# Kernel optimization log

Measured on AMD Instinct MI355X. Metric: run time of the kernel, lower is better.

## Reference

```python
import jax, jax.numpy as jnp
import numpy as np
from jax import lax

# ---- config (mirrors cfg) ----
NUM_LEVELS = 4
DS = 2            # DS_FACTOR
T = 16            # TILE_SIZE
SR = 4            # SEARCH_RADIUS
PADD = 1
SW = 0.1          # SPATIAL_WEIGHT
GR = 2            # GAUSS_RADIUS
SIGMA = 1.0
SS = 2 * (SR + PADD) + 1      # 11: padded search grid
SSC = 2 * SR + 1              # 9: cropped search grid
WIN = T + 2 * (SR + PADD)     # 26: gathered window per tile

# ---- subpixel-refinement quadratic-fit filters (from __init__) ----
F_A11 = jnp.asarray(np.array([[1,-2,1],[2,-4,2],[1,-2,1]], np.float32) / 4.0)
F_A22 = jnp.asarray(np.array([[1,2,1],[-2,-4,-2],[1,2,1]], np.float32) / 4.0)
F_A12 = jnp.asarray(np.array([[1,0,-1],[0,0,0],[-1,0,1]], np.float32) / 4.0)
F_B1  = jnp.asarray(np.array([[-1,0,1],[-2,0,2],[-1,0,1]], np.float32) / 8.0)
F_B2  = jnp.asarray(np.array([[-1,-2,-1],[0,0,0],[1,2,1]], np.float32) / 8.0)
F_C   = jnp.asarray(np.array([[-1,2,-1],[2,12,2],[-1,2,-1]], np.float32) / 16.0)


def _gauss_kernel():
    ws = 2 * GR + 1
    ax = np.arange(ws, dtype=np.float32) - GR
    g = np.exp(-(ax ** 2) / (2.0 * SIGMA ** 2))
    k = np.outer(g, g)
    k = k / k.sum()
    return jnp.asarray(k, jnp.float32)


def _pyramid(x):
    """Gaussian pyramid: depthwise gaussian blur + avg-pool(ds) per level."""
    k = _gauss_kernel()[None, None]  # OIHW, C=1
    pad = (2 * GR + 1 - 1) // 2
    pyr = [x]
    for _ in range(NUM_LEVELS - 1):
        y = lax.conv_general_dilated(x, k, (1, 1), [(pad, pad), (pad, pad)],
                                     dimension_numbers=('NCHW', 'OIHW', 'NCHW'))
        n, c, h, w = y.shape
        x = y.reshape(n, c, h // DS, DS, w // DS, DS).mean(axis=(3, 5))
        pyr.append(x)
    return pyr


def _sdist_map():
    ax = (np.arange(SS, dtype=np.float32) - (SR + PADD)) / float(SS)
    return jnp.asarray(ax[:, None] ** 2 + ax[None, :] ** 2, jnp.float32)


def _step(init_offset, src, dst):
    """One pyramid-level block-matching step + subpixel refine."""
    n, nth, ntw, _ = init_offset.shape
    H, W = src.shape[2], src.shape[3]
    oy = jnp.round(init_offset[..., 0]).astype(jnp.int32)
    ox = jnp.round(init_offset[..., 1]).astype(jnp.int32)
    base_y = (jnp.arange(nth, dtype=jnp.int32) * T)[None, :, None]
    base_x = (jnp.arange(ntw, dtype=jnp.int32) * T)[None, None, :]
    y0 = base_y + oy - (SR + PADD)
    x0 = base_x + ox - (SR + PADD)
    Y = jnp.clip(y0[..., None] + jnp.arange(WIN), 0, H - 1)
    X = jnp.clip(x0[..., None] + jnp.arange(WIN), 0, W - 1)
    nidx = jnp.arange(n)[:, None, None, None, None]
    window = dst[:, 0][nidx, Y[..., :, None], X[..., None, :]]
    # source tiles [n,nth,ntw,T,T]
    src_t = src[:, 0].reshape(n, nth, T, ntw, T).transpose(0, 1, 3, 2, 4)
    # all SSxSS candidate tiles from the window (static slide indices)
    sl = jnp.arange(SS)[:, None] + jnp.arange(T)[None, :]  # [SS,T]
    cand = window[:, :, :, sl[:, None, :, None], sl[None, :, None, :]]  # [n,nth,ntw,SS,SS,T,T]
    adist = jnp.mean((cand - src_t[:, :, :, None, None]) ** 2, axis=(-2, -1))
    dist_full = adist + SW * _sdist_map()  # [n,nth,ntw,SS,SS]
    dist = dist_full[:, :, :, PADD:-PADD, PADD:-PADD].reshape(n, nth, ntw, SSC * SSC)
    min_dist = jnp.min(dist, axis=3)
    pk = jnp.argmin(dist, axis=3)
    py = pk // SSC
    px = pk % SSC
    offset = init_offset + jnp.stack([(py - SR).astype(jnp.float32),
                                      (px - SR).astype(jnp.float32)], axis=3)
    # RegionSelection: 3x3 neighborhood of dist_full around (py+PADD, px+PADD)
    ry = (py + PADD)[..., None] + jnp.arange(-1, 2)
    rx = (px + PADD)[..., None] + jnp.arange(-1, 2)
    tyi = jnp.arange(nth)[None, :, None, None, None]
    txi = jnp.arange(ntw)[None, None, :, None, None]
    yreg = dist_full[nidx, tyi, txi, ry[..., :, None], rx[..., None, :]]  # [n,nth,ntw,3,3]
    s = lambda f: jnp.sum(f * yreg, axis=(-2, -1))
    a11 = jax.nn.relu(s(F_A11))
    a22 = jax.nn.relu(s(F_A22))
    a12 = s(F_A12)
    b1 = s(F_B1)
    b2 = s(F_B2)
    det = a11 * a22 - a12 ** 2
    a12z = jnp.where(det < 0, jnp.zeros_like(a12), a12)
    mu_x = -(a22 * b1 - a12z * b2) / det
    mu_y = -(a11 * b2 - a12z * b1) / det
    mu_len = jnp.sqrt(mu_y ** 2 + mu_x ** 2)
    dx = jnp.where(mu_len < 1.0, mu_x, jnp.zeros_like(mu_x))
    dy = jnp.where(mu_len < 1.0, mu_y, jnp.zeros_like(mu_y))
    offset = offset.at[..., 0].add(dy).at[..., 1].add(dx)
    return offset, min_dist


def _inherit(prev_offset, nth, ntw, H, W):
    typ = jnp.arange(nth) // DS
    txp = jnp.arange(ntw) // DS
    off = DS * prev_offset[:, typ[:, None], txp[None, :], :]
    iy = (jnp.arange(nth, dtype=jnp.float32) * T)[None, :, None]
    ix = (jnp.arange(ntw, dtype=jnp.float32) * T)[None, None, :]
    dy = jnp.clip(off[..., 0] + iy, 0.0, float(H - T)) - iy
    dx = jnp.clip(off[..., 1] + ix, 0.0, float(W - T)) - ix
    return jnp.round(jnp.stack([dy, dx], axis=3))


def _align(src, dst):
    ps = _pyramid(src)
    pd = _pyramid(dst)
    offset = None
    min_dist = None
    for level in range(NUM_LEVELS - 1, -1, -1):
        s, d = ps[level], pd[level]
        n, _, h, w = s.shape
        nth = int(np.ceil(h / T))
        ntw = int(np.ceil(w / T))
        if level == NUM_LEVELS - 1:
            init = jnp.zeros((n, nth, ntw, 2), jnp.float32)
        else:
            init = _inherit(offset, nth, ntw, h, w)
        offset, min_dist = _step(init, s, d)
    # nearest-neighbor upsample by TILE_SIZE to per-pixel maps
    pixel_off = jnp.repeat(jnp.repeat(offset, T, axis=1), T, axis=2)   # [n,H,W,2]
    pixel_dist = jnp.repeat(jnp.repeat(min_dist, T, axis=1), T, axis=2)  # [n,H,W]
    return pixel_off, pixel_dist


def setup_inputs() -> dict:
    key = jax.random.key(0)
    k1, k2 = jax.random.split(key)
    src = jax.random.uniform(k1, (4, 1, 512, 512), jnp.float32)
    dst = jax.random.uniform(k2, (4, 1, 512, 512), jnp.float32)
    return {"src": src, "dst": dst}


def reference(src, dst):
    return _align(src, dst)
```

## Files before the change

kernel.cpp:

```cpp
#include <hip/hip_runtime.h>


#define NB 4
#define NPIX (NB * 512 * 512)

constexpr float H6[6] = {
    0.027244342f, 0.149345013f, 0.323410645f,
    0.323410645f, 0.149345013f, 0.027244342f
};

__global__ void __launch_bounds__(256, 4)
pyramid_kernel(const float* __restrict__ src, const float* __restrict__ dst,
               float* __restrict__ ws) {
    __shared__ float smem[5520];
    float* patch = smem;
    float* tmpH1 = smem + 3840;
    float* l1    = smem;
    float* tmpH2 = smem + 784;
    float* l2    = smem + 1120;
    float* tmpH3 = smem + 1264;

    float* sL1 = ws;
    float* dL1 = sL1 + 4 * 65536;
    float* sL2 = dL1 + 4 * 65536;
    float* dL2 = sL2 + 4 * 16384;
    float* sL3 = dL2 + 4 * 16384;
    float* dL3 = sL3 + 4 * 4096;

    const int bx = blockIdx.x, by = blockIdx.y, z = blockIdx.z;
    const int t = threadIdx.x;
    const float* in = (z < 4) ? (src + (size_t)z * 262144) : (dst + (size_t)(z - 4) * 262144);
    float* oL1 = ((z < 4) ? sL1 : dL1) + (size_t)(z & 3) * 65536;
    float* oL2 = ((z < 4) ? sL2 : dL2) + (size_t)(z & 3) * 16384;
    float* oL3 = ((z < 4) ? sL3 : dL3) + (size_t)(z & 3) * 4096;

    {
        const int oy = by * 32 - 14, ox = bx * 32 - 14;
        for (int idx = t; idx < 3600; idx += 256) {
            int r = idx / 60, c = idx - r * 60;
            int gy = oy + r, gx = ox + c;
            float v = 0.f;
            if ((unsigned)gy < 512u && (unsigned)gx < 512u) v = in[gy * 512 + gx];
            patch[r * 64 + c] = v;
        }
    }
    __syncthreads();
    for (int idx = t; idx < 1680; idx += 256) {
        int r = idx / 28, v = idx - r * 28;
        const float* p = &patch[r * 64 + 2 * v];
        float a = 0.f;
        #pragma unroll
        for (int bq = 0; bq < 6; ++bq) a = fmaf(H6[bq], p[bq], a);
        tmpH1[r * 28 + v] = a;
    }
    __syncthreads();
    {
        const int oy = by * 16 - 6, ox = bx * 16 - 6;
        for (int idx = t; idx < 784; idx += 256) {
            int u = idx / 28, v = idx - u * 28;
            float a = 0.f;
            int y1 = oy + u, x1 = ox + v;
            if ((unsigned)y1 < 256u && (unsigned)x1 < 256u) {
                #pragma unroll
                for (int bq = 0; bq < 6; ++bq) a = fmaf(H6[bq], tmpH1[(2 * u + bq) * 28 + v], a);
            }
            l1[u * 28 + v] = a;
        }
    }
    __syncthreads();
    {
        int u = t >> 4, v = t & 15;
        oL1[(by * 16 + u) * 256 + bx * 16 + v] = l1[(6 + u) * 28 + 6 + v];
    }
    for (int idx = t; idx < 336; idx += 256) {
        int r = idx / 12, v = idx - r * 12;
        const float* p = &l1[r * 28 + 2 * v];
        float a = 0.f;
        #pragma unroll
        for (int bq = 0; bq < 6; ++bq) a = fmaf(H6[bq], p[bq], a);
        tmpH2[r * 12 + v] = a;
    }
    __syncthreads();
    {
        const int oy = by * 8 - 2, ox = bx * 8 - 2;
        if (t < 144) {
            int u = t / 12, v = t - u * 12;
            float a = 0.f;
            int y2 = oy + u, x2 = ox + v;
            if ((unsigned)y2 < 128u && (unsigned)x2 < 128u) {
                #pragma unroll
                for (int bq = 0; bq < 6; ++bq) a = fmaf(H6[bq], tmpH2[(2 * u + bq) * 12 + v], a);
            }
            l2[u * 12 + v] = a;
        }
    }
    __syncthreads();
    if (t < 64) {
        int u = t >> 3, v = t & 7;
        oL2[(by * 8 + u) * 128 + bx * 8 + v] = l2[(2 + u) * 12 + 2 + v];
    } else if (t < 112) {
        int idx = t - 64;
        int r = idx >> 2, v = idx & 3;
        const float* p = &l2[r * 12 + 2 * v];
        float a = 0.f;
        #pragma unroll
        for (int bq = 0; bq < 6; ++bq) a = fmaf(H6[bq], p[bq], a);
        tmpH3[r * 4 + v] = a;
    }
    __syncthreads();
    if (t < 16) {
        int u = t >> 2, v = t & 3;
        float a = 0.f;
        #pragma unroll
        for (int bq = 0; bq < 6; ++bq) a = fmaf(H6[bq], tmpH3[(2 * u + bq) * 4 + v], a);
        oL3[(by * 4 + u) * 64 + bx * 4 + v] = a;
    }
}

template<int NL>
__device__ __forceinline__ void do_level(const float* __restrict__ simg,
                                         const float* __restrict__ dimg, int H,
                                         int ty, int tx, float pary, float parx, bool first,
                                         float* win, float* st, float* dist, int lt,
                                         float& roy, float& rox, float& rod) {
    constexpr int ROWS = (NL == 128) ? 2 : 1;
    constexpr int G    = (NL == 128) ? 8 : 16;

    float dyf = 0.f, dxf = 0.f;
    if (!first) {
        float iy = (float)(ty * 16), ix = (float)(tx * 16);
        dyf = rintf(fminf(fmaxf(2.f * pary + iy, 0.f), (float)(H - 16)) - iy);
        dxf = rintf(fminf(fmaxf(2.f * parx + ix, 0.f), (float)(H - 16)) - ix);
    }
    const int ioy = (int)dyf, iox = (int)dxf;
    const int y0 = ty * 16 + ioy - 5;
    const int x0 = tx * 16 + iox - 5;

    for (int idx = lt; idx < 676; idx += NL) {
        int r = idx / 26, c = idx - r * 26;
        int gy = min(max(y0 + r, 0), H - 1);
        int gx = min(max(x0 + c, 0), H - 1);
        win[r * 28 + c] = dimg[gy * H + gx];
    }
    if (lt < 64) {
        int r = lt >> 2, q = lt & 3;
        const float4* srow = (const float4*)(simg + (size_t)(ty * 16 + r) * H + tx * 16);
        ((float4*)&st[r * 16])[q] = srow[q];
    }
    __syncthreads();

    const int dy = lt / G;
    if (dy < 11) {
        float acc[11];
        #pragma unroll
        for (int q = 0; q < 11; ++q) acc[q] = 0.f;
        #pragma unroll
        for (int rr = 0; rr < ROWS; ++rr) {
            const int i = (NL == 128) ? ((lt & 7) * 2 + rr) : (lt & 15);
            float w[28], s[16];
            const float4* wp = (const float4*)&win[(dy + i) * 28];
            #pragma unroll
            for (int q = 0; q < 7; ++q) ((float4*)w)[q] = wp[q];
            const float4* sp = (const float4*)&st[i * 16];
            #pragma unroll
            for (int q = 0; q < 4; ++q) ((float4*)s)[q] = sp[q];
            #pragma unroll
            for (int dx = 0; dx < 11; ++dx) {
                #pragma unroll
                for (int j = 0; j < 16; ++j) {
                    float d = w[dx + j] - s[j];
                    acc[dx] = fmaf(d, d, acc[dx]);
                }
            }
        }
        #pragma unroll
        for (int m = 1; m <= G / 2; m <<= 1) {
            #pragma unroll
            for (int dx = 0; dx < 11; ++dx) acc[dx] += __shfl_xor(acc[dx], m);
        }
        if ((lt & (G - 1)) == 0) {
            float ay = (float)(dy - 5) * (1.f / 11.f);
            #pragma unroll
            for (int dx = 0; dx < 11; ++dx) {
                float ax = (float)(dx - 5) * (1.f / 11.f);
                dist[dy * 11 + dx] = acc[dx] * (1.f / 256.f) + 0.1f * (ay * ay + ax * ax);
            }
        }
    }
    __syncthreads();

    const int l = lt & 63;
    float bv; int bk;
    {
        int k = l;
        int py = k / 9, px = k - (k / 9) * 9;
        bv = dist[(py + 1) * 11 + (px + 1)]; bk = k;
        k = l + 64;
        if (k < 81) {
            py = k / 9; px = k - (k / 9) * 9;
            float d = dist[(py + 1) * 11 + (px + 1)];
            if (d < bv) { bv = d; bk = k; }
        }
    }
    #pragma unroll
    for (int m = 1; m <= 32; m <<= 1) {
        float ov = __shfl_xor(bv, m);
        int   ok = __shfl_xor(bk, m);
        if (ov < bv || (ov == bv && ok < bk)) { bv = ov; bk = ok; }
    }
    {
        int py = bk / 9, px = bk - (bk / 9) * 9;
        float y00 = dist[(py + 0) * 11 + (px + 0)], y01 = dist[(py + 0) * 11 + (px + 1)], y02 = dist[(py + 0) * 11 + (px + 2)];
        float y10 = dist[(py + 1) * 11 + (px + 0)], y11 = dist[(py + 1) * 11 + (px + 1)], y12 = dist[(py + 1) * 11 + (px + 2)];
        float y20 = dist[(py + 2) * 11 + (px + 0)], y21 = dist[(py + 2) * 11 + (px + 1)], y22 = dist[(py + 2) * 11 + (px + 2)];

        float a11 = (y00 - 2.f * y01 + y02 + 2.f * y10 - 4.f * y11 + 2.f * y12 + y20 - 2.f * y21 + y22) * 0.25f;
        a11 = fmaxf(a11, 0.f);
        float a22 = (y00 + 2.f * y01 + y02 - 2.f * y10 - 4.f * y11 - 2.f * y12 + y20 + 2.f * y21 + y22) * 0.25f;
        a22 = fmaxf(a22, 0.f);
        float a12 = (y00 - y02 - y20 + y22) * 0.25f;
        float b1  = (-y00 + y02 - 2.f * y10 + 2.f * y12 - y20 + y22) * 0.125f;
        float b2  = (-y00 - 2.f * y01 - y02 + y20 + 2.f * y21 + y22) * 0.125f;

        float det  = a11 * a22 - a12 * a12;
        float a12z = (det < 0.f) ? 0.f : a12;
        float mu_x = -(a22 * b1 - a12z * b2) / det;
        float mu_y = -(a11 * b2 - a12z * b1) / det;
        float mu_len = sqrtf(mu_x * mu_x + mu_y * mu_y);
        float addx = (mu_len < 1.f) ? mu_x : 0.f;
        float addy = (mu_len < 1.f) ? mu_y : 0.f;

        roy = dyf + (float)(py - 4) + addy;
        rox = dxf + (float)(px - 4) + addx;
        rod = bv;
    }
}

__global__ void __launch_bounds__(512, 4)
step_chain_kernel(const float* __restrict__ src, const float* __restrict__ dst,
                  const float* __restrict__ ws, float* __restrict__ out) {
    __shared__ float smem[4448];

    const float* sL1 = ws;
    const float* dL1 = sL1 + 4 * 65536;
    const float* sL2 = dL1 + 4 * 65536;
    const float* dL2 = sL2 + 4 * 16384;
    const float* sL3 = dL2 + 4 * 16384;
    const float* dL3 = sL3 + 4 * 4096;

    const int gid = blockIdx.x;
    const int b   = gid >> 8;
    const int ty1 = (gid >> 4) & 15;
    const int tx1 = gid & 15;
    const int t    = threadIdx.x;
    const int slot = t >> 7;
    const int s_t  = t & 127;

    float* win0  = smem;
    float* st0   = smem + 2912;
    float* dist0 = smem + 3936;
    float* winH  = smem + slot * 728;
    float* stH   = smem + 2912 + slot * 256;
    float* distH = smem + 3936 + slot * 128;

    const float* s0 = src + (size_t)b * 262144; const float* d0 = dst + (size_t)b * 262144;
    const float* s1 = sL1 + (size_t)b * 65536;  const float* d1 = dL1 + (size_t)b * 65536;
    const float* s2 = sL2 + (size_t)b * 16384;  const float* d2 = dL2 + (size_t)b * 16384;
    const float* s3 = sL3 + (size_t)b * 4096;   const float* d3 = dL3 + (size_t)b * 4096;

    float oy, ox, od;
    do_level<512>(s3, d3,  64, ty1 >> 2, tx1 >> 2, 0.f, 0.f, true,
                  win0, st0, dist0, t, oy, ox, od);
    do_level<512>(s2, d2, 128, ty1 >> 1, tx1 >> 1, oy, ox, false,
                  win0, st0, dist0, t, oy, ox, od);
    do_level<512>(s1, d1, 256, ty1,      tx1,      oy, ox, false,
                  win0, st0, dist0, t, oy, ox, od);

    const int ty0 = 2 * ty1 + (slot >> 1), tx0 = 2 * tx1 + (slot & 1);
    do_level<128>(s0, d0, 512, ty0, tx0, oy, ox, false,
                  winH, stH, distH, s_t, oy, ox, od);

    int r = s_t >> 3, c = (s_t & 7) * 2;
    int pyy = ty0 * 16 + r, pxx = tx0 * 16 + c;
    size_t pi = ((size_t)(b * 512 + pyy)) * 512 + pxx;
    float2 o; o.x = oy; o.y = ox;
    ((float2*)out)[pi]     = o;
    ((float2*)out)[pi + 1] = o;
    float2 dd; dd.x = od; dd.y = od;
    *(float2*)(out + (size_t)NPIX * 2 + pi) = dd;
}

extern "C" void kernel_launch(void* const* d_in, const int* in_sizes, int n_in,
                              void* d_out, int out_size, void* d_ws, size_t ws_size,
                              hipStream_t stream) {
    const float* src = (const float*)d_in[0];
    const float* dst = (const float*)d_in[1];
    float* out = (float*)d_out;
    float* ws  = (float*)d_ws;

    hipLaunchKernelGGL(pyramid_kernel, dim3(16, 16, 8), dim3(256), 0, stream, src, dst, ws);
    hipLaunchKernelGGL(step_chain_kernel, dim3(1024), dim3(512), 0, stream, src, dst, ws, out);
}
```

Before: 117.4 us.

## Run one level-0 tile per 128-thread block, recomputing coarse levels redundantly

The step chain kernel now launches 4096 blocks of 128 threads, one per finest-level tile. Each block redundantly recomputes the coarse levels 3, 2 and 1 for its own ancestor tiles, instead of 512-thread blocks sharing those levels and splitting level 0 across four slots. The aim is more and smaller blocks with less shared memory, for better occupancy and less barrier cost. The cost is roughly four times the coarse-level work, and the coarse levels now use the 2-rows-per-thread path.

```diff
diff --git a/kernel.cpp b/kernel.cpp
--- a/kernel.cpp
+++ b/kernel.cpp
@@ -117,15 +117,11 @@
     }
 }
 
-template<int NL>
 __device__ __forceinline__ void do_level(const float* __restrict__ simg,
                                          const float* __restrict__ dimg, int H,
                                          int ty, int tx, float pary, float parx, bool first,
                                          float* win, float* st, float* dist, int lt,
                                          float& roy, float& rox, float& rod) {
-    constexpr int ROWS = (NL == 128) ? 2 : 1;
-    constexpr int G    = (NL == 128) ? 8 : 16;
-
     float dyf = 0.f, dxf = 0.f;
     if (!first) {
         float iy = (float)(ty * 16), ix = (float)(tx * 16);
@@ -136,7 +132,7 @@
     const int y0 = ty * 16 + ioy - 5;
     const int x0 = tx * 16 + iox - 5;
 
-    for (int idx = lt; idx < 676; idx += NL) {
+    for (int idx = lt; idx < 676; idx += 128) {
         int r = idx / 26, c = idx - r * 26;
         int gy = min(max(y0 + r, 0), H - 1);
         int gx = min(max(x0 + c, 0), H - 1);
@@ -149,14 +145,14 @@
     }
     __syncthreads();
 
-    const int dy = lt / G;
+    const int dy = lt >> 3;
     if (dy < 11) {
         float acc[11];
         #pragma unroll
         for (int q = 0; q < 11; ++q) acc[q] = 0.f;
         #pragma unroll
-        for (int rr = 0; rr < ROWS; ++rr) {
-            const int i = (NL == 128) ? ((lt & 7) * 2 + rr) : (lt & 15);
+        for (int rr = 0; rr < 2; ++rr) {
+            const int i = (lt & 7) * 2 + rr;
             float w[28], s[16];
             const float4* wp = (const float4*)&win[(dy + i) * 28];
             #pragma unroll
@@ -174,11 +170,11 @@
             }
         }
         #pragma unroll
-        for (int m = 1; m <= G / 2; m <<= 1) {
+        for (int m = 1; m <= 4; m <<= 1) {
             #pragma unroll
             for (int dx = 0; dx < 11; ++dx) acc[dx] += __shfl_xor(acc[dx], m);
         }
-        if ((lt & (G - 1)) == 0) {
+        if ((lt & 7) == 0) {
             float ay = (float)(dy - 5) * (1.f / 11.f);
             #pragma unroll
             for (int dx = 0; dx < 11; ++dx) {
@@ -236,10 +232,13 @@
     }
 }
 
-__global__ void __launch_bounds__(512, 4)
+__global__ void __launch_bounds__(128, 8)
 step_chain_kernel(const float* __restrict__ src, const float* __restrict__ dst,
                   const float* __restrict__ ws, float* __restrict__ out) {
-    __shared__ float smem[4448];
+    __shared__ float smem[1112];
+    float* win  = smem;
+    float* st   = smem + 728;
+    float* dist = smem + 984;
 
     const float* sL1 = ws;
     const float* dL1 = sL1 + 4 * 65536;
@@ -249,19 +248,10 @@
     const float* dL3 = sL3 + 4 * 4096;
 
     const int gid = blockIdx.x;
-    const int b   = gid >> 8;
-    const int ty1 = (gid >> 4) & 15;
-    const int tx1 = gid & 15;
-    const int t    = threadIdx.x;
-    const int slot = t >> 7;
-    const int s_t  = t & 127;
-
-    float* win0  = smem;
-    float* st0   = smem + 2912;
-    float* dist0 = smem + 3936;
-    float* winH  = smem + slot * 728;
-    float* stH   = smem + 2912 + slot * 256;
-    float* distH = smem + 3936 + slot * 128;
+    const int b   = gid >> 10;
+    const int ty0 = (gid >> 5) & 31;
+    const int tx0 = gid & 31;
+    const int t   = threadIdx.x;
 
     const float* s0 = src + (size_t)b * 262144; const float* d0 = dst + (size_t)b * 262144;
     const float* s1 = sL1 + (size_t)b * 65536;  const float* d1 = dL1 + (size_t)b * 65536;
@@ -269,18 +259,16 @@
     const float* s3 = sL3 + (size_t)b * 4096;   const float* d3 = dL3 + (size_t)b * 4096;
 
     float oy, ox, od;
-    do_level<512>(s3, d3,  64, ty1 >> 2, tx1 >> 2, 0.f, 0.f, true,
-                  win0, st0, dist0, t, oy, ox, od);
-    do_level<512>(s2, d2, 128, ty1 >> 1, tx1 >> 1, oy, ox, false,
-                  win0, st0, dist0, t, oy, ox, od);
-    do_level<512>(s1, d1, 256, ty1,      tx1,      oy, ox, false,
-                  win0, st0, dist0, t, oy, ox, od);
-
-    const int ty0 = 2 * ty1 + (slot >> 1), tx0 = 2 * tx1 + (slot & 1);
-    do_level<128>(s0, d0, 512, ty0, tx0, oy, ox, false,
-                  winH, stH, distH, s_t, oy, ox, od);
-
-    int r = s_t >> 3, c = (s_t & 7) * 2;
+    do_level(s3, d3,  64, ty0 >> 3, tx0 >> 3, 0.f, 0.f, true,
+             win, st, dist, t, oy, ox, od);
+    do_level(s2, d2, 128, ty0 >> 2, tx0 >> 2, oy, ox, false,
+             win, st, dist, t, oy, ox, od);
+    do_level(s1, d1, 256, ty0 >> 1, tx0 >> 1, oy, ox, false,
+             win, st, dist, t, oy, ox, od);
+    do_level(s0, d0, 512, ty0,      tx0,      oy, ox, false,
+             win, st, dist, t, oy, ox, od);
+
+    int r = t >> 3, c = (t & 7) * 2;
     int pyy = ty0 * 16 + r, pxx = tx0 * 16 + c;
     size_t pi = ((size_t)(b * 512 + pyy)) * 512 + pxx;
     float2 o; o.x = oy; o.y = ox;
@@ -299,5 +287,5 @@
     float* ws  = (float*)d_ws;
 
     hipLaunchKernelGGL(pyramid_kernel, dim3(16, 16, 8), dim3(256), 0, stream, src, dst, ws);
-    hipLaunchKernelGGL(step_chain_kernel, dim3(1024), dim3(512), 0, stream, src, dst, ws, out);
-}
+    hipLaunchKernelGGL(step_chain_kernel, dim3(4096), dim3(128), 0, stream, src, dst, ws, out);
+}
```

After: 191.3 us. 1.63x slower.
